# Kernel optimization log

Measured on AMD Instinct MI355X. Metric: run time of the kernel, lower is better.

## Reference

```python
import jax, jax.numpy as jnp
import numpy as np

MAX_STEP = 20

def setup_inputs() -> dict:
    key = jax.random.key(0)
    k1, k2 = jax.random.split(key)
    B, L, E, H = 32, 2048, 256, 256
    word_rep = jax.random.normal(k1, (B, L, E), dtype=jnp.float32)
    # nn.Parameter(torch.randn(...).uniform_(-0.1, 0.1)) -> uniform in [-0.1, 0.1]
    cnn = jax.random.uniform(k2, (MAX_STEP, E, H), dtype=jnp.float32, minval=-0.1, maxval=0.1)
    return {"word_rep": word_rep, "cnn": cnn}

def reference(word_rep, cnn):
    # word_rep: [B, L, E]; cnn: [MAX_STEP, E, H]
    L = word_rep.shape[1]
    # Gather the cyclically-indexed per-position weight: [L, E, H]
    W = cnn[jnp.arange(L) % MAX_STEP]
    # Fused batched matmul over all positions at once: [B, L, H]
    hidden_vecs = jnp.einsum('ble,leh->blh', word_rep, W)
    return (hidden_vecs, hidden_vecs[:, -1])
```

## Files before the change

### kernel.cpp

```cpp
#include <hip/hip_runtime.h>
#include <hip/hip_bf16.h>

#define B_ 32
#define L_ 2048
#define E_ 256
#define H_ 256
#define MAXSTEP 20
#define NLW 4
#define NCH 26
#define NGRP (MAXSTEP * NCH)

typedef __attribute__((ext_vector_type(4))) float f32x4;
typedef __attribute__((ext_vector_type(8))) short bf16x8;
using bf16 = __hip_bfloat16;

__device__ inline short cvt1(float x) {
    bf16 b = __float2bfloat16(x);
    return *reinterpret_cast<short*>(&b);
}

__global__ void transpose_w_kernel(const float* __restrict__ cnn, short* __restrict__ wt) {
    __shared__ short tile[32][33];
    const int s  = blockIdx.z;
    const int e0 = blockIdx.y * 32;
    const int h0 = blockIdx.x * 32;
    const int tx = threadIdx.x;
    const int ty = threadIdx.y;
    const float* src = cnn + ((size_t)s * E_ + e0) * H_ + h0;
#pragma unroll
    for (int i = ty; i < 32; i += 8)
        tile[i][tx] = cvt1(src[(size_t)i * H_ + tx]);
    __syncthreads();
    short* dst = wt + ((size_t)s * H_ + h0) * E_ + e0;
#pragma unroll
    for (int i = ty; i < 32; i += 8)
        dst[(size_t)i * E_ + tx] = tile[tx][i];
}

__global__ __launch_bounds__(64, 4) void vaw_wave_kernel(
        const float* __restrict__ A, const short* __restrict__ Wt,
        float* __restrict__ out) {
    __shared__ __align__(16) float aLds[3][B_ * 64];

    const int p     = blockIdx.x;
    const int xcd   = p & 7;
    const int slot  = p >> 3;
    const int g_    = xcd + 8 * (slot >> 2);
    const int cg    = slot & 3;
    const int s     = g_ / NCH;
    const int chunk = g_ % NCH;
    const int cnt   = (s < 8) ? 103 : 102;
    const int lane  = threadIdx.x;
    const int r     = lane & 15;
    const int g     = lane >> 4;
    const int nbase = cg * 64;
    const int key   = r & 7;

    auto lof = [&](int il) {
        int idx = chunk * NLW + il;
        if (idx > cnt - 1) idx = cnt - 1;
        return s + 20 * idx;
    };

    auto stage = [&](int td) {
        const int l  = lof(td >> 2);
        const int kq = td & 3;
        float* dst = aLds[td % 3];
        const int row = (lane >> 4);
        const int cL  = lane & 15;
#pragma unroll
        for (int j = 0; j < 8; ++j) {
            const int rr = j * 4 + row;
            const int cG = cL ^ (rr & 7);
            const float* gp = A + ((size_t)rr * L_ + l) * E_ + kq * 64 + cG * 4;
            __builtin_amdgcn_global_load_lds(
                (const __attribute__((address_space(1))) void*)gp,
                (__attribute__((address_space(3))) void*)&dst[j * 4 * 64],
                16, 0, 0);
        }
    };

    stage(0);
    stage(1);

    const short* wtb = Wt + ((size_t)s * H_ + nbase + r) * E_ + g * 8;
    bf16x8 breg[8][4];
#pragma unroll
    for (int kk = 0; kk < 8; ++kk)
#pragma unroll
        for (int nf = 0; nf < 4; ++nf)
            breg[kk][nf] = *(const bf16x8*)(wtb + (size_t)nf * 16 * E_ + kk * 32);

    f32x4 acc[2][4];

#pragma unroll 1
    for (int il = 0; il < NLW; ++il) {
        const int l      = lof(il);
        const bool first = (il == 0);
        const bool last  = (il == NLW - 1);

#pragma unroll
        for (int q = 0; q < 4; ++q) {
            const int t   = il * 4 + q;
            const int buf = t % 3;

            if (!last || q < 2) stage(t + 2);

            if (q == 0) {
                asm volatile("s_waitcnt vmcnt(48)" ::: "memory");
            } else if (q == 1) {
                asm volatile("s_waitcnt vmcnt(48)" ::: "memory");
            } else if (q == 2) {
                if (last)  asm volatile("s_waitcnt vmcnt(8)"  ::: "memory");
                else       asm volatile("s_waitcnt vmcnt(16)" ::: "memory");
            } else {
                if (last)  asm volatile("s_waitcnt vmcnt(0)"  ::: "memory");
                else       asm volatile("s_waitcnt vmcnt(16)" ::: "memory");
            }
            __builtin_amdgcn_sched_barrier(0);

            if (q == 0) {
#pragma unroll
                for (int mf = 0; mf < 2; ++mf)
#pragma unroll
                    for (int nf = 0; nf < 4; ++nf)
                        acc[mf][nf] = f32x4{0.f, 0.f, 0.f, 0.f};
            }

#pragma unroll
            for (int kkh = 0; kkh < 2; ++kkh) {
                const int kk = q * 2 + kkh;
                const int c0 = kkh * 8 + g * 2;
                f32x4 a0lo = *(const f32x4*)&aLds[buf][r * 64 + ((c0 ^ key) << 2)];
                f32x4 a0hi = *(const f32x4*)&aLds[buf][r * 64 + (((c0 + 1) ^ key) << 2)];
                f32x4 a1lo = *(const f32x4*)&aLds[buf][(r + 16) * 64 + ((c0 ^ key) << 2)];
                f32x4 a1hi = *(const f32x4*)&aLds[buf][(r + 16) * 64 + (((c0 + 1) ^ key) << 2)];
                bf16x8 a0, a1;
#pragma unroll
                for (int j = 0; j < 4; ++j) {
                    a0[j]     = cvt1(a0lo[j]);
                    a0[j + 4] = cvt1(a0hi[j]);
                    a1[j]     = cvt1(a1lo[j]);
                    a1[j + 4] = cvt1(a1hi[j]);
                }
#pragma unroll
                for (int nf = 0; nf < 4; ++nf) {
                    acc[0][nf] = __builtin_amdgcn_mfma_f32_16x16x32_bf16(a0, breg[kk][nf], acc[0][nf], 0, 0, 0);
                    acc[1][nf] = __builtin_amdgcn_mfma_f32_16x16x32_bf16(a1, breg[kk][nf], acc[1][nf], 0, 0, 0);
                }
            }

            if (q == 3) {
                const int row0 = g * 4;
#pragma unroll
                for (int mf = 0; mf < 2; ++mf) {
#pragma unroll
                    for (int nf = 0; nf < 4; ++nf) {
                        const int h = nbase + nf * 16 + r;
#pragma unroll
                        for (int i = 0; i < 4; ++i) {
                            const int bb = mf * 16 + row0 + i;
                            out[((size_t)bb * L_ + l) * H_ + h] = acc[mf][nf][i];
                        }
                    }
                }
                if (l == L_ - 1) {
                    float* out2 = out + (size_t)B_ * L_ * H_;
#pragma unroll
                    for (int mf = 0; mf < 2; ++mf)
#pragma unroll
                        for (int nf = 0; nf < 4; ++nf) {
                            const int h = nbase + nf * 16 + r;
#pragma unroll
                            for (int i = 0; i < 4; ++i) {
                                const int bb = mf * 16 + row0 + i;
                                out2[(size_t)bb * H_ + h] = acc[mf][nf][i];
                            }
                        }
                }
            }
        }
    }
}

__global__ __launch_bounds__(256) void vaw_fallback_kernel(
        const float* __restrict__ A, const float* __restrict__ W, float* __restrict__ out) {
    __shared__ __align__(16) float aLds[2][B_ * E_];
    const int l0   = blockIdx.x * 4;
    const int wv   = threadIdx.x >> 6;
    const int lane = threadIdx.x & 63;
    const int r    = lane & 15;
    const int g    = lane >> 4;
    const int nbase = wv * 64;
    const int key   = r & 7;

    auto stage = [&](int it) {
        float* dst = aLds[it & 1];
        const int l = l0 + it;
#pragma unroll
        for (int t = 0; t < 8; ++t) {
            const int b  = t * 4 + wv;
            const int cgx = lane ^ (b & 7);
            const float* gp = A + ((size_t)b * L_ + l) * E_ + cgx * 4;
            __builtin_amdgcn_global_load_lds(
                (const __attribute__((address_space(1))) void*)gp,
                (__attribute__((address_space(3))) void*)&dst[b * 256],
                16, 0, 0);
        }
    };

    stage(0);
#pragma unroll 1
    for (int it = 0; it < 4; ++it) {
        const int l   = l0 + it;
        const int sidx = l % MAXSTEP;
        const int cur = it & 1;
        if (it < 3) {
            stage(it + 1);
            asm volatile("s_waitcnt vmcnt(8)" ::: "memory");
        } else {
            asm volatile("s_waitcnt vmcnt(0)" ::: "memory");
        }
        __builtin_amdgcn_s_barrier();
        __builtin_amdgcn_sched_barrier(0);

        f32x4 acc[2][4] = {};
        const float* Wf = W + (size_t)sidx * E_ * H_;
#pragma unroll 2
        for (int kk = 0; kk < 8; ++kk) {
            const int k0 = kk * 32;
            const int c0 = kk * 8 + g * 2;
            f32x4 a0lo = *(const f32x4*)&aLds[cur][r * 256 + ((c0 ^ key) << 2)];
            f32x4 a0hi = *(const f32x4*)&aLds[cur][r * 256 + (((c0 + 1) ^ key) << 2)];
            f32x4 a1lo = *(const f32x4*)&aLds[cur][(r + 16) * 256 + ((c0 ^ key) << 2)];
            f32x4 a1hi = *(const f32x4*)&aLds[cur][(r + 16) * 256 + (((c0 + 1) ^ key) << 2)];
            bf16x8 a0, a1;
#pragma unroll
            for (int j = 0; j < 4; ++j) {
                a0[j]     = cvt1(a0lo[j]);
                a0[j + 4] = cvt1(a0hi[j]);
                a1[j]     = cvt1(a1lo[j]);
                a1[j + 4] = cvt1(a1hi[j]);
            }
            bf16x8 b0, b1, b2, b3;
#pragma unroll
            for (int j = 0; j < 8; ++j) {
                const size_t krow = (size_t)(k0 + g * 8 + j) * H_;
                b0[j] = cvt1(Wf[krow + nbase +  0 + r]);
                b1[j] = cvt1(Wf[krow + nbase + 16 + r]);
                b2[j] = cvt1(Wf[krow + nbase + 32 + r]);
                b3[j] = cvt1(Wf[krow + nbase + 48 + r]);
            }
            acc[0][0] = __builtin_amdgcn_mfma_f32_16x16x32_bf16(a0, b0, acc[0][0], 0, 0, 0);
            acc[0][1] = __builtin_amdgcn_mfma_f32_16x16x32_bf16(a0, b1, acc[0][1], 0, 0, 0);
            acc[0][2] = __builtin_amdgcn_mfma_f32_16x16x32_bf16(a0, b2, acc[0][2], 0, 0, 0);
            acc[0][3] = __builtin_amdgcn_mfma_f32_16x16x32_bf16(a0, b3, acc[0][3], 0, 0, 0);
            acc[1][0] = __builtin_amdgcn_mfma_f32_16x16x32_bf16(a1, b0, acc[1][0], 0, 0, 0);
            acc[1][1] = __builtin_amdgcn_mfma_f32_16x16x32_bf16(a1, b1, acc[1][1], 0, 0, 0);
            acc[1][2] = __builtin_amdgcn_mfma_f32_16x16x32_bf16(a1, b2, acc[1][2], 0, 0, 0);
            acc[1][3] = __builtin_amdgcn_mfma_f32_16x16x32_bf16(a1, b3, acc[1][3], 0, 0, 0);
        }

        const int row0 = g * 4;
#pragma unroll
        for (int mf = 0; mf < 2; ++mf)
#pragma unroll
            for (int nf = 0; nf < 4; ++nf) {
                const int h = nbase + nf * 16 + r;
#pragma unroll
                for (int i = 0; i < 4; ++i) {
                    const int bb = mf * 16 + row0 + i;
                    out[((size_t)bb * L_ + l) * H_ + h] = acc[mf][nf][i];
                }
            }
        if (l == L_ - 1) {
            float* out2 = out + (size_t)B_ * L_ * H_;
#pragma unroll
            for (int mf = 0; mf < 2; ++mf)
#pragma unroll
                for (int nf = 0; nf < 4; ++nf) {
                    const int h = nbase + nf * 16 + r;
#pragma unroll
                    for (int i = 0; i < 4; ++i) {
                        const int bb = mf * 16 + row0 + i;
                        out2[(size_t)bb * H_ + h] = acc[mf][nf][i];
                    }
                }
        }
        __builtin_amdgcn_s_barrier();
    }
}

extern "C" void kernel_launch(void* const* d_in, const int* in_sizes, int n_in,
                              void* d_out, int out_size, void* d_ws, size_t ws_size,
                              hipStream_t stream) {
    const float* word_rep = (const float*)d_in[0];
    const float* cnn      = (const float*)d_in[1];
    float* out = (float*)d_out;

    const size_t wt_bytes = (size_t)MAXSTEP * E_ * H_ * sizeof(short);
    if (ws_size >= wt_bytes) {
        short* wt = (short*)d_ws;
        transpose_w_kernel<<<dim3(8, 8, 20), dim3(32, 8), 0, stream>>>(cnn, wt);
        vaw_wave_kernel<<<dim3(NGRP * 4), dim3(64), 0, stream>>>(word_rep, wt, out);
    } else {
        vaw_fallback_kernel<<<dim3(L_ / 4), dim3(256), 0, stream>>>(word_rep, cnn, out);
    }
}
```

Baseline: 45.49 us.

## Replace LDS-staged A tiles with direct register double-buffered loads in 4-wave blocks

The main kernel no longer stages activation tiles through shared memory with async global-to-LDS loads and hand-tuned waitcnts. Each wave now loads its own A fragments straight into registers, double-buffered one k-step ahead. Four waves (one per H quarter) are packed into a 256-thread block over the same position group. The XCD-aware block remapping is dropped. This removes the LDS round trip and the manual vmcnt tuning, but it leaves only one k-step of prefetch depth. Each wave also now issues redundant global loads of the same A rows that the other waves read, relying on cache for reuse.

```diff
diff --git a/kernel.cpp b/kernel.cpp
--- a/kernel.cpp
+++ b/kernel.cpp
@@ -37,51 +37,38 @@
         dst[(size_t)i * E_ + tx] = tile[tx][i];
 }
 
-__global__ __launch_bounds__(64, 4) void vaw_wave_kernel(
+__global__ __launch_bounds__(256, 2) void vaw_reg_kernel(
         const float* __restrict__ A, const short* __restrict__ Wt,
         float* __restrict__ out) {
-    __shared__ __align__(16) float aLds[3][B_ * 64];
-
-    const int p     = blockIdx.x;
-    const int xcd   = p & 7;
-    const int slot  = p >> 3;
-    const int g_    = xcd + 8 * (slot >> 2);
-    const int cg    = slot & 3;
+    const int g_    = blockIdx.x;
     const int s     = g_ / NCH;
     const int chunk = g_ % NCH;
     const int cnt   = (s < 8) ? 103 : 102;
-    const int lane  = threadIdx.x;
+    const int wv    = threadIdx.x >> 6;
+    const int lane  = threadIdx.x & 63;
     const int r     = lane & 15;
     const int g     = lane >> 4;
-    const int nbase = cg * 64;
-    const int key   = r & 7;
-
-    auto lof = [&](int il) {
+    const int nbase = wv * 64;
+
+    int lv[NLW];
+#pragma unroll
+    for (int il = 0; il < NLW; ++il) {
         int idx = chunk * NLW + il;
         if (idx > cnt - 1) idx = cnt - 1;
-        return s + 20 * idx;
+        lv[il] = s + 20 * idx;
+    }
+
+    auto loadk = [&](f32x4* dst, int l, int kk) {
+        const float* p0 = A + ((size_t)r * L_ + l) * E_ + g * 8 + kk * 32;
+        const float* p1 = A + ((size_t)(r + 16) * L_ + l) * E_ + g * 8 + kk * 32;
+        dst[0] = *(const f32x4*)p0;
+        dst[1] = *(const f32x4*)(p0 + 4);
+        dst[2] = *(const f32x4*)p1;
+        dst[3] = *(const f32x4*)(p1 + 4);
     };
 
-    auto stage = [&](int td) {
-        const int l  = lof(td >> 2);
-        const int kq = td & 3;
-        float* dst = aLds[td % 3];
-        const int row = (lane >> 4);
-        const int cL  = lane & 15;
-#pragma unroll
-        for (int j = 0; j < 8; ++j) {
-            const int rr = j * 4 + row;
-            const int cG = cL ^ (rr & 7);
-            const float* gp = A + ((size_t)rr * L_ + l) * E_ + kq * 64 + cG * 4;
-            __builtin_amdgcn_global_load_lds(
-                (const __attribute__((address_space(1))) void*)gp,
-                (__attribute__((address_space(3))) void*)&dst[j * 4 * 64],
-                16, 0, 0);
-        }
-    };
-
-    stage(0);
-    stage(1);
+    f32x4 abuf[2][4];
+    loadk(abuf[0], lv[0], 0);
 
     const short* wtb = Wt + ((size_t)s * H_ + nbase + r) * E_ + g * 8;
     bf16x8 breg[8][4];
@@ -91,94 +78,67 @@
         for (int nf = 0; nf < 4; ++nf)
             breg[kk][nf] = *(const bf16x8*)(wtb + (size_t)nf * 16 * E_ + kk * 32);
 
-    f32x4 acc[2][4];
-
-#pragma unroll 1
+#pragma unroll
     for (int il = 0; il < NLW; ++il) {
-        const int l      = lof(il);
-        const bool first = (il == 0);
-        const bool last  = (il == NLW - 1);
-
-#pragma unroll
-        for (int q = 0; q < 4; ++q) {
-            const int t   = il * 4 + q;
-            const int buf = t % 3;
-
-            if (!last || q < 2) stage(t + 2);
-
-            if (q == 0) {
-                asm volatile("s_waitcnt vmcnt(48)" ::: "memory");
-            } else if (q == 1) {
-                asm volatile("s_waitcnt vmcnt(48)" ::: "memory");
-            } else if (q == 2) {
-                if (last)  asm volatile("s_waitcnt vmcnt(8)"  ::: "memory");
-                else       asm volatile("s_waitcnt vmcnt(16)" ::: "memory");
-            } else {
-                if (last)  asm volatile("s_waitcnt vmcnt(0)"  ::: "memory");
-                else       asm volatile("s_waitcnt vmcnt(16)" ::: "memory");
+        const int l = lv[il];
+        f32x4 acc[2][4];
+#pragma unroll
+        for (int mf = 0; mf < 2; ++mf)
+#pragma unroll
+            for (int nf = 0; nf < 4; ++nf)
+                acc[mf][nf] = f32x4{0.f, 0.f, 0.f, 0.f};
+
+#pragma unroll
+        for (int kk = 0; kk < 8; ++kk) {
+            const int t  = il * 8 + kk;
+            const int cb = t & 1;
+            if (t < NLW * 8 - 1) {
+                const int tn = t + 1;
+                loadk(abuf[cb ^ 1], lv[tn >> 3], tn & 7);
             }
             __builtin_amdgcn_sched_barrier(0);
 
-            if (q == 0) {
-#pragma unroll
-                for (int mf = 0; mf < 2; ++mf)
-#pragma unroll
-                    for (int nf = 0; nf < 4; ++nf)
-                        acc[mf][nf] = f32x4{0.f, 0.f, 0.f, 0.f};
-            }
-
-#pragma unroll
-            for (int kkh = 0; kkh < 2; ++kkh) {
-                const int kk = q * 2 + kkh;
-                const int c0 = kkh * 8 + g * 2;
-                f32x4 a0lo = *(const f32x4*)&aLds[buf][r * 64 + ((c0 ^ key) << 2)];
-                f32x4 a0hi = *(const f32x4*)&aLds[buf][r * 64 + (((c0 + 1) ^ key) << 2)];
-                f32x4 a1lo = *(const f32x4*)&aLds[buf][(r + 16) * 64 + ((c0 ^ key) << 2)];
-                f32x4 a1hi = *(const f32x4*)&aLds[buf][(r + 16) * 64 + (((c0 + 1) ^ key) << 2)];
-                bf16x8 a0, a1;
-#pragma unroll
-                for (int j = 0; j < 4; ++j) {
-                    a0[j]     = cvt1(a0lo[j]);
-                    a0[j + 4] = cvt1(a0hi[j]);
-                    a1[j]     = cvt1(a1lo[j]);
-                    a1[j + 4] = cvt1(a1hi[j]);
-                }
+            bf16x8 a0, a1;
+#pragma unroll
+            for (int j = 0; j < 4; ++j) {
+                a0[j]     = cvt1(abuf[cb][0][j]);
+                a0[j + 4] = cvt1(abuf[cb][1][j]);
+                a1[j]     = cvt1(abuf[cb][2][j]);
+                a1[j + 4] = cvt1(abuf[cb][3][j]);
+            }
+#pragma unroll
+            for (int nf = 0; nf < 4; ++nf) {
+                acc[0][nf] = __builtin_amdgcn_mfma_f32_16x16x32_bf16(a0, breg[kk][nf], acc[0][nf], 0, 0, 0);
+                acc[1][nf] = __builtin_amdgcn_mfma_f32_16x16x32_bf16(a1, breg[kk][nf], acc[1][nf], 0, 0, 0);
+            }
+        }
+
+        const int row0 = g * 4;
+#pragma unroll
+        for (int mf = 0; mf < 2; ++mf) {
+#pragma unroll
+            for (int nf = 0; nf < 4; ++nf) {
+                const int h = nbase + nf * 16 + r;
+#pragma unroll
+                for (int i = 0; i < 4; ++i) {
+                    const int bb = mf * 16 + row0 + i;
+                    out[((size_t)bb * L_ + l) * H_ + h] = acc[mf][nf][i];
+                }
+            }
+        }
+        if (l == L_ - 1) {
+            float* out2 = out + (size_t)B_ * L_ * H_;
+#pragma unroll
+            for (int mf = 0; mf < 2; ++mf)
 #pragma unroll
                 for (int nf = 0; nf < 4; ++nf) {
-                    acc[0][nf] = __builtin_amdgcn_mfma_f32_16x16x32_bf16(a0, breg[kk][nf], acc[0][nf], 0, 0, 0);
-                    acc[1][nf] = __builtin_amdgcn_mfma_f32_16x16x32_bf16(a1, breg[kk][nf], acc[1][nf], 0, 0, 0);
-                }
-            }
-
-            if (q == 3) {
-                const int row0 = g * 4;
-#pragma unroll
-                for (int mf = 0; mf < 2; ++mf) {
-#pragma unroll
-                    for (int nf = 0; nf < 4; ++nf) {
-                        const int h = nbase + nf * 16 + r;
-#pragma unroll
-                        for (int i = 0; i < 4; ++i) {
-                            const int bb = mf * 16 + row0 + i;
-                            out[((size_t)bb * L_ + l) * H_ + h] = acc[mf][nf][i];
-                        }
+                    const int h = nbase + nf * 16 + r;
+#pragma unroll
+                    for (int i = 0; i < 4; ++i) {
+                        const int bb = mf * 16 + row0 + i;
+                        out2[(size_t)bb * H_ + h] = acc[mf][nf][i];
                     }
                 }
-                if (l == L_ - 1) {
-                    float* out2 = out + (size_t)B_ * L_ * H_;
-#pragma unroll
-                    for (int mf = 0; mf < 2; ++mf)
-#pragma unroll
-                        for (int nf = 0; nf < 4; ++nf) {
-                            const int h = nbase + nf * 16 + r;
-#pragma unroll
-                            for (int i = 0; i < 4; ++i) {
-                                const int bb = mf * 16 + row0 + i;
-                                out2[(size_t)bb * H_ + h] = acc[mf][nf][i];
-                            }
-                        }
-                }
-            }
         }
     }
 }
@@ -302,7 +262,7 @@
     if (ws_size >= wt_bytes) {
         short* wt = (short*)d_ws;
         transpose_w_kernel<<<dim3(8, 8, 20), dim3(32, 8), 0, stream>>>(cnn, wt);
-        vaw_wave_kernel<<<dim3(NGRP * 4), dim3(64), 0, stream>>>(word_rep, wt, out);
+        vaw_reg_kernel<<<dim3(NGRP), dim3(256), 0, stream>>>(word_rep, wt, out);
     } else {
         vaw_fallback_kernel<<<dim3(L_ / 4), dim3(256), 0, stream>>>(word_rep, cnn, out);
     }
```

Measured after the change: 73.85 us. +62.3%, slower.
